# Kernel tuning notes

Hardware: AMD Instinct MI355X
Metric: run time of the kernel (lower is better)

## Reference

```python
import jax, jax.numpy as jnp
import numpy as np

B, TF, TP = 32, 2048, 256
FRAME_DIM, PHN_DIM, ATT_DIM = 768, 512, 512
LN_EPS = 1e-5


def setup_inputs() -> dict:
    key = jax.random.key(0)
    ks = jax.random.split(key, 9)
    frame_hidden = jax.random.normal(ks[0], (B, TF, FRAME_DIM), dtype=jnp.float32)
    phn_hidden = jax.random.normal(ks[1], (B, TP, PHN_DIM), dtype=jnp.float32)
    labels_att_mask = jax.random.randint(ks[2], (B, TP), 0, 2, dtype=jnp.int32)
    # ensure every row has at least one attended phoneme position
    labels_att_mask = labels_att_mask.at[:, 0].set(1)
    s_q = 1.0 / np.sqrt(FRAME_DIM)
    s_k = 1.0 / np.sqrt(PHN_DIM)
    Wq = jax.random.uniform(ks[3], (FRAME_DIM, ATT_DIM), jnp.float32, -s_q, s_q)
    bq = jax.random.uniform(ks[4], (ATT_DIM,), jnp.float32, -s_q, s_q)
    Wk = jax.random.uniform(ks[5], (PHN_DIM, ATT_DIM), jnp.float32, -s_k, s_k)
    bk = jax.random.uniform(ks[6], (ATT_DIM,), jnp.float32, -s_k, s_k)
    gamma = jnp.ones((2 * ATT_DIM,), jnp.float32)
    beta = jnp.zeros((2 * ATT_DIM,), jnp.float32)
    return {"frame_hidden": frame_hidden, "phn_hidden": phn_hidden,
            "labels_att_mask": labels_att_mask,
            "Wq": Wq, "bq": bq, "Wk": Wk, "bk": bk,
            "gamma": gamma, "beta": beta}


def _layer_norm(x, gamma, beta):
    mu = jnp.mean(x, axis=-1, keepdims=True)
    var = jnp.mean(jnp.square(x - mu), axis=-1, keepdims=True)
    return (x - mu) * jax.lax.rsqrt(var + LN_EPS) * gamma + beta


def reference(frame_hidden, phn_hidden, labels_att_mask, Wq, bq, Wk, bk, gamma, beta):
    q_frame = jnp.einsum('btf,fa->bta', frame_hidden, Wq) + bq   # [B,TF,A]
    k_phn = jnp.einsum('bpf,fa->bpa', phn_hidden, Wk) + bk       # [B,TP,A]
    energy = jnp.einsum('bta,bpa->btp', q_frame, k_phn)          # unscaled QK^T
    att_mask = (1.0 - labels_att_mask.astype(energy.dtype)) * -1000.0  # [B,TP]
    energy = energy + att_mask[:, None, :]
    att_matrix = jax.nn.softmax(energy, axis=-1)
    att_out = jnp.einsum('btp,bpa->bta', att_matrix, k_phn)      # [B,TF,A]
    att_out = jnp.concatenate([att_out, q_frame], axis=-1)       # [B,TF,2A]
    att_out = _layer_norm(att_out, gamma, beta)
    return (att_out, energy)
```

## Files before the change

kernel.cpp:

```cpp
#include <hip/hip_runtime.h>


typedef __bf16 bf16x8 __attribute__((ext_vector_type(8)));
typedef float  f32x4  __attribute__((ext_vector_type(4)));
typedef int    i32x4  __attribute__((ext_vector_type(4)));
typedef int    i32x2  __attribute__((ext_vector_type(2)));
typedef unsigned short u16;

__device__ __forceinline__ u16 f2b(float f) {
  union { float f; unsigned int i; } v; v.f = f;
  unsigned int u = v.i;
  return (u16)((u + 0x7FFFu + ((u >> 16) & 1u)) >> 16);
}
__device__ __forceinline__ float b2f(u16 u) {
  union { unsigned int i; float f; } v; v.i = ((unsigned int)u) << 16; return v.f;
}
__device__ __forceinline__ bf16x8 ldfrag(const u16* p) {
  return __builtin_bit_cast(bf16x8, *(const i32x4*)p);
}
__device__ __forceinline__ f32x4 mfma16(bf16x8 a, bf16x8 b, f32x4 c) {
  return __builtin_amdgcn_mfma_f32_16x16x32_bf16(a, b, c, 0, 0, 0);
}

__global__ void transpose_f32_bf16(const float* __restrict__ in, u16* __restrict__ out,
                                   int R, int C) {
  __shared__ u16 tile[32][33];
  int c0 = blockIdx.x * 32, r0 = blockIdx.y * 32;
  int x = threadIdx.x, y = threadIdx.y;
#pragma unroll
  for (int i = 0; i < 32; i += 8) tile[y + i][x] = f2b(in[(size_t)(r0 + y + i) * C + c0 + x]);
  __syncthreads();
#pragma unroll
  for (int i = 0; i < 32; i += 8) out[(size_t)(c0 + y + i) * R + r0 + x] = tile[x][y + i];
}

__global__ void transpose_bf16(const u16* __restrict__ in, u16* __restrict__ out,
                               int R, int C, long inStride, long outStride) {
  __shared__ u16 tile[32][33];
  long bb = blockIdx.z;
  in  += bb * inStride;
  out += bb * outStride;
  int c0 = blockIdx.x * 32, r0 = blockIdx.y * 32;
  int x = threadIdx.x, y = threadIdx.y;
#pragma unroll
  for (int i = 0; i < 32; i += 8) tile[y + i][x] = in[(size_t)(r0 + y + i) * C + c0 + x];
  __syncthreads();
#pragma unroll
  for (int i = 0; i < 32; i += 8) out[(size_t)(c0 + y + i) * R + r0 + x] = tile[x][y + i];
}

__global__ __launch_bounds__(256, 2) void gemm_bias_bt(
    const float* __restrict__ A, const u16* __restrict__ Bt,
    const float* __restrict__ bias, u16* __restrict__ C, int M, int N, int K) {
  __shared__ u16 As[128][72];
  __shared__ u16 Bs[128][72];
  int tid = threadIdx.x, wave = tid >> 6, lane = tid & 63;
  int l = lane & 15, q = lane >> 4;
  int wr = wave >> 1, wc = wave & 1;
  int m0 = blockIdx.y * 128, n0 = blockIdx.x * 128;
  int aRow = tid >> 4, aCol = (tid & 15) * 4;
  int bRow = tid >> 3, bCol = (tid & 7) * 8;

  f32x4 acc[4][4];
#pragma unroll
  for (int mt = 0; mt < 4; mt++)
#pragma unroll
    for (int nt = 0; nt < 4; nt++) acc[mt][nt] = (f32x4)0.0f;

  for (int kc = 0; kc < K; kc += 64) {
    __syncthreads();
#pragma unroll
    for (int i = 0; i < 8; i++) {
      int r = aRow + i * 16;
      f32x4 v = *(const f32x4*)&A[(size_t)(m0 + r) * K + kc + aCol];
      u16 t[4];
#pragma unroll
      for (int j = 0; j < 4; j++) t[j] = f2b(v[j]);
      *(i32x2*)&As[r][aCol] = *(i32x2*)t;
    }
#pragma unroll
    for (int i = 0; i < 4; i++) {
      int r = bRow + i * 32;
      *(i32x4*)&Bs[r][bCol] = *(const i32x4*)&Bt[(size_t)(n0 + r) * K + kc + bCol];
    }
    __syncthreads();
#pragma unroll
    for (int ks = 0; ks < 64; ks += 32) {
      bf16x8 af[4], bv[4];
#pragma unroll
      for (int mt = 0; mt < 4; mt++) af[mt] = ldfrag(&As[wr * 64 + mt * 16 + l][ks + q * 8]);
#pragma unroll
      for (int nt = 0; nt < 4; nt++) bv[nt] = ldfrag(&Bs[wc * 64 + nt * 16 + l][ks + q * 8]);
#pragma unroll
      for (int mt = 0; mt < 4; mt++)
#pragma unroll
        for (int nt = 0; nt < 4; nt++) acc[mt][nt] = mfma16(af[mt], bv[nt], acc[mt][nt]);
    }
  }
#pragma unroll
  for (int nt = 0; nt < 4; nt++) {
    int col = n0 + wc * 64 + nt * 16 + l;
    float bvv = bias[col];
#pragma unroll
    for (int mt = 0; mt < 4; mt++)
#pragma unroll
      for (int r = 0; r < 4; r++) {
        int row = m0 + wr * 64 + mt * 16 + q * 4 + r;
        C[(size_t)row * N + col] = f2b(acc[mt][nt][r] + bvv);
      }
  }
}

__global__ __launch_bounds__(256, 2) void attn_fused(
    const u16* __restrict__ Qbuf,
    const u16* __restrict__ Kp,
    const u16* __restrict__ KpT,
    const int* __restrict__ mask,
    const float* __restrict__ gamma, const float* __restrict__ beta,
    float* __restrict__ out0,
    float* __restrict__ out1) {
  __shared__ __align__(16) char smem[54272];
  u16* Qs  = (u16*)(smem);
  u16* Ks  = (u16*)(smem + 9216);
  u16* Ps  = (u16*)(smem);
  u16* Kts = (u16*)(smem + 33792);

  int tid = threadIdx.x, wave = tid >> 6, lane = tid & 63;
  int l = lane & 15, q = lane >> 4;
  int m0 = blockIdx.x * 64, b = blockIdx.y;
  const u16* Qb  = Qbuf + ((size_t)b * 2048 + m0) * 512;
  const u16* Kb  = Kp  + (size_t)b * 256 * 512;
  const u16* KTb = KpT + (size_t)b * 512 * 256;

  float madd[16];
#pragma unroll
  for (int nt = 0; nt < 16; nt++)
    madd[nt] = (float)(1 - mask[b * 256 + nt * 16 + l]) * -1000.0f;

  f32x4 accE[16];
#pragma unroll
  for (int nt = 0; nt < 16; nt++) accE[nt] = (f32x4)0.0f;
  int ldRow = tid >> 3, ldCol = (tid & 7) * 8;
  for (int kc = 0; kc < 512; kc += 64) {
    __syncthreads();
#pragma unroll
    for (int i = 0; i < 2; i++) {
      int r = ldRow + i * 32;
      *(i32x4*)&Qs[r * 72 + ldCol] = *(const i32x4*)&Qb[(size_t)r * 512 + kc + ldCol];
    }
#pragma unroll
    for (int i = 0; i < 8; i++) {
      int r = ldRow + i * 32;
      *(i32x4*)&Ks[r * 72 + ldCol] = *(const i32x4*)&Kb[(size_t)r * 512 + kc + ldCol];
    }
    __syncthreads();
#pragma unroll
    for (int ks = 0; ks < 64; ks += 32) {
      bf16x8 af = ldfrag(&Qs[(wave * 16 + l) * 72 + ks + q * 8]);
#pragma unroll
      for (int nt = 0; nt < 16; nt++) {
        bf16x8 bv = ldfrag(&Ks[(nt * 16 + l) * 72 + ks + q * 8]);
        accE[nt] = mfma16(af, bv, accE[nt]);
      }
    }
  }

  int rbase = m0 + wave * 16 + q * 4;
#pragma unroll
  for (int nt = 0; nt < 16; nt++)
#pragma unroll
    for (int r = 0; r < 4; r++) accE[nt][r] += madd[nt];

#pragma unroll
  for (int r = 0; r < 4; r++) {
    size_t rowoff = ((size_t)b * 2048 + rbase + r) * 256;
#pragma unroll
    for (int nt = 0; nt < 16; nt++) out1[rowoff + nt * 16 + l] = accE[nt][r];
  }

  float mx[4], sm[4], rs[4];
#pragma unroll
  for (int r = 0; r < 4; r++) mx[r] = -1e30f;
#pragma unroll
  for (int nt = 0; nt < 16; nt++)
#pragma unroll
    for (int r = 0; r < 4; r++) mx[r] = fmaxf(mx[r], accE[nt][r]);
#pragma unroll
  for (int off = 1; off < 16; off <<= 1)
#pragma unroll
    for (int r = 0; r < 4; r++) mx[r] = fmaxf(mx[r], __shfl_xor(mx[r], off));
#pragma unroll
  for (int r = 0; r < 4; r++) sm[r] = 0.0f;
#pragma unroll
  for (int nt = 0; nt < 16; nt++)
#pragma unroll
    for (int r = 0; r < 4; r++) {
      float p = __expf(accE[nt][r] - mx[r]);
      accE[nt][r] = p;
      sm[r] += p;
    }
#pragma unroll
  for (int off = 1; off < 16; off <<= 1)
#pragma unroll
    for (int r = 0; r < 4; r++) sm[r] += __shfl_xor(sm[r], off);
#pragma unroll
  for (int r = 0; r < 4; r++) rs[r] = 1.0f / sm[r];

  __syncthreads();
#pragma unroll
  for (int r = 0; r < 4; r++)
#pragma unroll
    for (int nt = 0; nt < 16; nt++)
      Ps[(wave * 16 + q * 4 + r) * 264 + nt * 16 + l] = f2b(accE[nt][r] * rs[r]);

  f32x4 accO[32];
#pragma unroll
  for (int g = 0; g < 32; g++) accO[g] = (f32x4)0.0f;
  for (int h = 0; h < 2; h++) {
    for (int pc = 0; pc < 256; pc += 32) {
      __syncthreads();
#pragma unroll
      for (int i = 0; i < 4; i++) {
        int r = (tid >> 2) + i * 64, c = (tid & 3) * 8;
        *(i32x4*)&Kts[r * 40 + c] =
            *(const i32x4*)&KTb[(size_t)(h * 256 + r) * 256 + pc + c];
      }
      __syncthreads();
      bf16x8 af = ldfrag(&Ps[(wave * 16 + l) * 264 + pc + q * 8]);
#pragma unroll
      for (int nt = 0; nt < 16; nt++) {
        bf16x8 bv = ldfrag(&Kts[(nt * 16 + l) * 40 + q * 8]);
        accO[h * 16 + nt] = mfma16(af, bv, accO[h * 16 + nt]);
      }
    }
  }

  float s1[4], s2[4];
#pragma unroll
  for (int r = 0; r < 4; r++) { s1[r] = 0.0f; s2[r] = 0.0f; }
#pragma unroll
  for (int g = 0; g < 32; g++)
#pragma unroll
    for (int r = 0; r < 4; r++) { float v = accO[g][r]; s1[r] += v; s2[r] += v * v; }
#pragma unroll
  for (int r = 0; r < 4; r++) {
    const u16* qr = Qb + (size_t)(wave * 16 + q * 4 + r) * 512;
#pragma unroll
    for (int p = 0; p < 4; p++) {
      bf16x8 qv = ldfrag(&qr[p * 128 + l * 8]);
#pragma unroll
      for (int j = 0; j < 8; j++) { float v = (float)qv[j]; s1[r] += v; s2[r] += v * v; }
    }
  }
#pragma unroll
  for (int off = 1; off < 16; off <<= 1)
#pragma unroll
    for (int r = 0; r < 4; r++) {
      s1[r] += __shfl_xor(s1[r], off);
      s2[r] += __shfl_xor(s2[r], off);
    }
#pragma unroll
  for (int r = 0; r < 4; r++) {
    float mean = s1[r] * (1.0f / 1024.0f);
    float var  = s2[r] * (1.0f / 1024.0f) - mean * mean;
    float rstd = rsqrtf(var + 1e-5f);
    size_t rowbase = ((size_t)b * 2048 + rbase + r) * 1024;
#pragma unroll
    for (int g = 0; g < 32; g++) {
      int col = g * 16 + l;
      out0[rowbase + col] = (accO[g][r] - mean) * rstd * gamma[col] + beta[col];
    }
    const u16* qr = Qb + (size_t)(wave * 16 + q * 4 + r) * 512;
#pragma unroll
    for (int p = 0; p < 4; p++) {
      bf16x8 qv = ldfrag(&qr[p * 128 + l * 8]);
      float ov[8];
#pragma unroll
      for (int j = 0; j < 8; j++) {
        int col = 512 + p * 128 + l * 8 + j;
        ov[j] = ((float)qv[j] - mean) * rstd * gamma[col] + beta[col];
      }
      *(f32x4*)&out0[rowbase + 512 + p * 128 + l * 8] = *(f32x4*)&ov[0];
      *(f32x4*)&out0[rowbase + 516 + p * 128 + l * 8] = *(f32x4*)&ov[4];
    }
  }
}

extern "C" void kernel_launch(void* const* d_in, const int* in_sizes, int n_in,
                              void* d_out, int out_size, void* d_ws, size_t ws_size,
                              hipStream_t stream) {
  (void)in_sizes; (void)n_in; (void)out_size; (void)ws_size;
  const float* frame = (const float*)d_in[0];
  const float* phn   = (const float*)d_in[1];
  const int*   msk   = (const int*)d_in[2];
  const float* Wq    = (const float*)d_in[3];
  const float* bq    = (const float*)d_in[4];
  const float* Wk    = (const float*)d_in[5];
  const float* bk    = (const float*)d_in[6];
  const float* gamma = (const float*)d_in[7];
  const float* beta  = (const float*)d_in[8];

  u16* ws   = (u16*)d_ws;
  u16* WqT  = ws;
  u16* WkT  = ws + 393216;
  u16* Qbuf = ws + 655360;
  u16* Kp   = ws + 34209792;
  u16* KpT  = ws + 38404096;

  float* out0 = (float*)d_out;
  float* out1 = out0 + (size_t)32 * 2048 * 1024;

  transpose_f32_bf16<<<dim3(16, 24, 1), dim3(32, 8, 1), 0, stream>>>(Wq, WqT, 768, 512);
  transpose_f32_bf16<<<dim3(16, 16, 1), dim3(32, 8, 1), 0, stream>>>(Wk, WkT, 512, 512);
  gemm_bias_bt<<<dim3(4, 512, 1), dim3(256, 1, 1), 0, stream>>>(frame, WqT, bq, Qbuf, 65536, 512, 768);
  gemm_bias_bt<<<dim3(4, 64, 1), dim3(256, 1, 1), 0, stream>>>(phn, WkT, bk, Kp, 8192, 512, 512);
  transpose_bf16<<<dim3(16, 8, 32), dim3(32, 8, 1), 0, stream>>>(Kp, KpT, 256, 512, 131072, 131072);
  attn_fused<<<dim3(32, 32, 1), dim3(256, 1, 1), 0, stream>>>(Qbuf, Kp, KpT, msk, gamma, beta, out0, out1);
}
```

Before: 696.3 us.

## Double-buffer GEMM and attention loads with direct-to-LDS swizzled copies and XCD block swizzle

```diff
diff --git a/kernel.cpp b/kernel.cpp
--- a/kernel.cpp
+++ b/kernel.cpp
@@ -2,6 +2,7 @@
 
 
 typedef __bf16 bf16x8 __attribute__((ext_vector_type(8)));
+typedef __bf16 bf16x4 __attribute__((ext_vector_type(4)));
 typedef float  f32x4  __attribute__((ext_vector_type(4)));
 typedef int    i32x4  __attribute__((ext_vector_type(4)));
 typedef int    i32x2  __attribute__((ext_vector_type(2)));
@@ -12,14 +13,16 @@
   unsigned int u = v.i;
   return (u16)((u + 0x7FFFu + ((u >> 16) & 1u)) >> 16);
 }
-__device__ __forceinline__ float b2f(u16 u) {
-  union { unsigned int i; float f; } v; v.i = ((unsigned int)u) << 16; return v.f;
-}
 __device__ __forceinline__ bf16x8 ldfrag(const u16* p) {
   return __builtin_bit_cast(bf16x8, *(const i32x4*)p);
 }
 __device__ __forceinline__ f32x4 mfma16(bf16x8 a, bf16x8 b, f32x4 c) {
   return __builtin_amdgcn_mfma_f32_16x16x32_bf16(a, b, c, 0, 0, 0);
+}
+__device__ __forceinline__ void gl_lds16(const void* g, void* l) {
+  __builtin_amdgcn_global_load_lds(
+      (const __attribute__((address_space(1))) void*)g,
+      (__attribute__((address_space(3))) void*)l, 16, 0, 0);
 }
 
 __global__ void transpose_f32_bf16(const float* __restrict__ in, u16* __restrict__ out,
@@ -52,51 +55,80 @@
 __global__ __launch_bounds__(256, 2) void gemm_bias_bt(
     const float* __restrict__ A, const u16* __restrict__ Bt,
     const float* __restrict__ bias, u16* __restrict__ C, int M, int N, int K) {
-  __shared__ u16 As[128][72];
-  __shared__ u16 Bs[128][72];
+  __shared__ __align__(16) u16 As[2][128][72];
+  __shared__ __align__(16) u16 Bs[2][128][64];
   int tid = threadIdx.x, wave = tid >> 6, lane = tid & 63;
   int l = lane & 15, q = lane >> 4;
   int wr = wave >> 1, wc = wave & 1;
-  int m0 = blockIdx.y * 128, n0 = blockIdx.x * 128;
+
+  int chunk = gridDim.x >> 3;
+  int swz = (blockIdx.x & 7) * chunk + (blockIdx.x >> 3);
+  int n0 = (swz & 3) * 128, m0 = (swz >> 2) * 128;
+
   int aRow = tid >> 4, aCol = (tid & 15) * 4;
-  int bRow = tid >> 3, bCol = (tid & 7) * 8;
+  int NT = K >> 6;
+  int sw = ((lane & 7) ^ (lane >> 3)) << 4;
 
   f32x4 acc[4][4];
 #pragma unroll
   for (int mt = 0; mt < 4; mt++)
 #pragma unroll
     for (int nt = 0; nt < 4; nt++) acc[mt][nt] = (f32x4)0.0f;
-
-  for (int kc = 0; kc < K; kc += 64) {
-    __syncthreads();
+  f32x4 pf[8];
+
+  auto stageB = [&](int buf, int kc) {
+#pragma unroll
+    for (int i = 0; i < 4; i++) {
+      int rb = wave * 4 + i;
+      int r  = rb * 8 + (lane >> 3);
+      const char* src = (const char*)Bt + ((size_t)(n0 + r) * K + kc) * 2 + sw;
+      gl_lds16(src, (char*)&Bs[buf][0][0] + rb * 1024);
+    }
+  };
+  auto loadA = [&](int kc) {
+#pragma unroll
+    for (int i = 0; i < 8; i++)
+      pf[i] = *(const f32x4*)&A[(size_t)(m0 + aRow + i * 16) * K + kc + aCol];
+  };
+  auto writeA = [&](int buf) {
 #pragma unroll
     for (int i = 0; i < 8; i++) {
-      int r = aRow + i * 16;
-      f32x4 v = *(const f32x4*)&A[(size_t)(m0 + r) * K + kc + aCol];
-      u16 t[4];
-#pragma unroll
-      for (int j = 0; j < 4; j++) t[j] = f2b(v[j]);
-      *(i32x2*)&As[r][aCol] = *(i32x2*)t;
-    }
-#pragma unroll
-    for (int i = 0; i < 4; i++) {
-      int r = bRow + i * 32;
-      *(i32x4*)&Bs[r][bCol] = *(const i32x4*)&Bt[(size_t)(n0 + r) * K + kc + bCol];
-    }
-    __syncthreads();
+      bf16x4 h;
+#pragma unroll
+      for (int j = 0; j < 4; j++) h[j] = (__bf16)pf[i][j];
+      *(i32x2*)&As[buf][aRow + i * 16][aCol] = __builtin_bit_cast(i32x2, h);
+    }
+  };
+
+  stageB(0, 0);
+  loadA(0);
+  writeA(0);
+  __syncthreads();
+
+  for (int t = 0; t < NT; t++) {
+    int cur = t & 1, nxt = cur ^ 1;
+    bool more = (t + 1 < NT);
+    if (more) { stageB(nxt, (t + 1) << 6); loadA((t + 1) << 6); }
 #pragma unroll
     for (int ks = 0; ks < 64; ks += 32) {
       bf16x8 af[4], bv[4];
 #pragma unroll
-      for (int mt = 0; mt < 4; mt++) af[mt] = ldfrag(&As[wr * 64 + mt * 16 + l][ks + q * 8]);
-#pragma unroll
-      for (int nt = 0; nt < 4; nt++) bv[nt] = ldfrag(&Bs[wc * 64 + nt * 16 + l][ks + q * 8]);
+      for (int mt = 0; mt < 4; mt++) af[mt] = ldfrag(&As[cur][wr * 64 + mt * 16 + l][ks + q * 8]);
+#pragma unroll
+      for (int nt = 0; nt < 4; nt++) {
+        int row = wc * 64 + nt * 16 + l;
+        bv[nt] = ldfrag((const u16*)((const char*)&Bs[cur][0][0] + row * 128 +
+                                     (((ks << 1) + q * 16) ^ ((l & 7) << 4))));
+      }
 #pragma unroll
       for (int mt = 0; mt < 4; mt++)
 #pragma unroll
         for (int nt = 0; nt < 4; nt++) acc[mt][nt] = mfma16(af[mt], bv[nt], acc[mt][nt]);
     }
-  }
+    if (more) writeA(nxt);
+    __syncthreads();
+  }
+
 #pragma unroll
   for (int nt = 0; nt < 4; nt++) {
     int col = n0 + wc * 64 + nt * 16 + l;
@@ -119,51 +151,88 @@
     const float* __restrict__ gamma, const float* __restrict__ beta,
     float* __restrict__ out0,
     float* __restrict__ out1) {
-  __shared__ __align__(16) char smem[54272];
-  u16* Qs  = (u16*)(smem);
-  u16* Ks  = (u16*)(smem + 9216);
-  u16* Ps  = (u16*)(smem);
-  u16* Kts = (u16*)(smem + 33792);
+  __shared__ __align__(16) char smem[74752];
+  u16* Ps   = (u16*)smem;
+  u16* Kts0 = (u16*)(smem + 33792);
 
   int tid = threadIdx.x, wave = tid >> 6, lane = tid & 63;
   int l = lane & 15, q = lane >> 4;
-  int m0 = blockIdx.x * 64, b = blockIdx.y;
+
+  int chunk = gridDim.x >> 3;
+  int swz = (blockIdx.x & 7) * chunk + (blockIdx.x >> 3);
+  int m0 = (swz & 31) * 64, b = swz >> 5;
+
   const u16* Qb  = Qbuf + ((size_t)b * 2048 + m0) * 512;
   const u16* Kb  = Kp  + (size_t)b * 256 * 512;
   const u16* KTb = KpT + (size_t)b * 512 * 256;
+  int sw = ((lane & 7) ^ (lane >> 3)) << 4;
 
   float madd[16];
 #pragma unroll
   for (int nt = 0; nt < 16; nt++)
     madd[nt] = (float)(1 - mask[b * 256 + nt * 16 + l]) * -1000.0f;
 
+  bf16x8 af[16];
+#pragma unroll
+  for (int t = 0; t < 8; t++)
+#pragma unroll
+    for (int s = 0; s < 2; s++)
+      af[t * 2 + s] = ldfrag(&Qb[(size_t)(wave * 16 + l) * 512 + t * 64 + s * 32 + q * 8]);
+
+  auto stageK = [&](int buf, int kc) {
+#pragma unroll
+    for (int i = 0; i < 8; i++) {
+      int rb = wave * 8 + i;
+      int r  = rb * 8 + (lane >> 3);
+      const char* src = (const char*)Kb + ((size_t)r * 512 + kc) * 2 + sw;
+      gl_lds16(src, smem + buf * 32768 + rb * 1024);
+    }
+  };
+
   f32x4 accE[16];
 #pragma unroll
   for (int nt = 0; nt < 16; nt++) accE[nt] = (f32x4)0.0f;
-  int ldRow = tid >> 3, ldCol = (tid & 7) * 8;
-  for (int kc = 0; kc < 512; kc += 64) {
+
+  stageK(0, 0);
+  __syncthreads();
+#pragma unroll
+  for (int t = 0; t < 8; t++) {
+    int cur = t & 1;
+    if (t < 7) stageK(cur ^ 1, (t + 1) * 64);
+    const char* kb = smem + cur * 32768;
+    __builtin_amdgcn_s_setprio(1);
+#pragma unroll
+    for (int s = 0; s < 2; s++) {
+      bf16x8 a = af[t * 2 + s];
+#pragma unroll
+      for (int nt = 0; nt < 16; nt++) {
+        int row = nt * 16 + l;
+        bf16x8 bv = ldfrag((const u16*)(kb + row * 128 +
+                                        ((s * 64 + q * 16) ^ ((l & 7) << 4))));
+        accE[nt] = mfma16(a, bv, accE[nt]);
+      }
+    }
+    __builtin_amdgcn_s_setprio(0);
     __syncthreads();
-#pragma unroll
-    for (int i = 0; i < 2; i++) {
-      int r = ldRow + i * 32;
-      *(i32x4*)&Qs[r * 72 + ldCol] = *(const i32x4*)&Qb[(size_t)r * 512 + kc + ldCol];
-    }
-#pragma unroll
-    for (int i = 0; i < 8; i++) {
-      int r = ldRow + i * 32;
-      *(i32x4*)&Ks[r * 72 + ldCol] = *(const i32x4*)&Kb[(size_t)r * 512 + kc + ldCol];
-    }
-    __syncthreads();
-#pragma unroll
-    for (int ks = 0; ks < 64; ks += 32) {
-      bf16x8 af = ldfrag(&Qs[(wave * 16 + l) * 72 + ks + q * 8]);
-#pragma unroll
-      for (int nt = 0; nt < 16; nt++) {
-        bf16x8 bv = ldfrag(&Ks[(nt * 16 + l) * 72 + ks + q * 8]);
-        accE[nt] = mfma16(af, bv, accE[nt]);
-      }
-    }
-  }
+  }
+
+  i32x4 kpf[4];
+  auto loadKts = [&](int t) {
+    int h = t >> 3, pc = (t & 7) * 32;
+#pragma unroll
+    for (int i = 0; i < 4; i++) {
+      int r = (tid >> 2) + i * 64, c = (tid & 3) * 8;
+      kpf[i] = *(const i32x4*)&KTb[(size_t)(h * 256 + r) * 256 + pc + c];
+    }
+  };
+  auto writeKts = [&](int buf) {
+#pragma unroll
+    for (int i = 0; i < 4; i++) {
+      int r = (tid >> 2) + i * 64, c = (tid & 3) * 8;
+      *(i32x4*)&Kts0[(size_t)buf * 10240 + r * 40 + c] = kpf[i];
+    }
+  };
+  loadKts(0);
 
   int rbase = m0 + wave * 16 + q * 4;
 #pragma unroll
@@ -206,33 +275,32 @@
 #pragma unroll
   for (int r = 0; r < 4; r++) rs[r] = 1.0f / sm[r];
 
-  __syncthreads();
 #pragma unroll
   for (int r = 0; r < 4; r++)
 #pragma unroll
     for (int nt = 0; nt < 16; nt++)
       Ps[(wave * 16 + q * 4 + r) * 264 + nt * 16 + l] = f2b(accE[nt][r] * rs[r]);
 
+  writeKts(0);
+  __syncthreads();
+
   f32x4 accO[32];
 #pragma unroll
   for (int g = 0; g < 32; g++) accO[g] = (f32x4)0.0f;
-  for (int h = 0; h < 2; h++) {
-    for (int pc = 0; pc < 256; pc += 32) {
-      __syncthreads();
-#pragma unroll
-      for (int i = 0; i < 4; i++) {
-        int r = (tid >> 2) + i * 64, c = (tid & 3) * 8;
-        *(i32x4*)&Kts[r * 40 + c] =
-            *(const i32x4*)&KTb[(size_t)(h * 256 + r) * 256 + pc + c];
-      }
-      __syncthreads();
-      bf16x8 af = ldfrag(&Ps[(wave * 16 + l) * 264 + pc + q * 8]);
-#pragma unroll
-      for (int nt = 0; nt < 16; nt++) {
-        bf16x8 bv = ldfrag(&Kts[(nt * 16 + l) * 40 + q * 8]);
-        accO[h * 16 + nt] = mfma16(af, bv, accO[h * 16 + nt]);
-      }
-    }
+#pragma unroll
+  for (int t = 0; t < 16; t++) {
+    int cur = t & 1, h = t >> 3, pc = (t & 7) * 32;
+    if (t < 15) loadKts(t + 1);
+    bf16x8 ps = ldfrag(&Ps[(wave * 16 + l) * 264 + pc + q * 8]);
+    __builtin_amdgcn_s_setprio(1);
+#pragma unroll
+    for (int nt = 0; nt < 16; nt++) {
+      bf16x8 bv = ldfrag(&Kts0[(size_t)cur * 10240 + (nt * 16 + l) * 40 + q * 8]);
+      accO[h * 16 + nt] = mfma16(ps, bv, accO[h * 16 + nt]);
+    }
+    __builtin_amdgcn_s_setprio(0);
+    if (t < 15) writeKts(cur ^ 1);
+    __syncthreads();
   }
 
   float s1[4], s2[4];
@@ -312,8 +380,8 @@
 
   transpose_f32_bf16<<<dim3(16, 24, 1), dim3(32, 8, 1), 0, stream>>>(Wq, WqT, 768, 512);
   transpose_f32_bf16<<<dim3(16, 16, 1), dim3(32, 8, 1), 0, stream>>>(Wk, WkT, 512, 512);
-  gemm_bias_bt<<<dim3(4, 512, 1), dim3(256, 1, 1), 0, stream>>>(frame, WqT, bq, Qbuf, 65536, 512, 768);
-  gemm_bias_bt<<<dim3(4, 64, 1), dim3(256, 1, 1), 0, stream>>>(phn, WkT, bk, Kp, 8192, 512, 512);
+  gemm_bias_bt<<<dim3(2048, 1, 1), dim3(256, 1, 1), 0, stream>>>(frame, WqT, bq, Qbuf, 65536, 512, 768);
+  gemm_bias_bt<<<dim3(256, 1, 1), dim3(256, 1, 1), 0, stream>>>(phn, WkT, bk, Kp, 8192, 512, 512);
   transpose_bf16<<<dim3(16, 8, 32), dim3(32, 8, 1), 0, stream>>>(Kp, KpT, 256, 512, 131072, 131072);
-  attn_fused<<<dim3(32, 32, 1), dim3(256, 1, 1), 0, stream>>>(Qbuf, Kp, KpT, msk, gamma, beta, out0, out1);
-}
+  attn_fused<<<dim3(1024, 1, 1), dim3(256, 1, 1), 0, stream>>>(Qbuf, Kp, KpT, msk, gamma, beta, out0, out1);
+}
```

Result: faster. 670.8 us (-3.7%).
